# Optimization experiments

Hardware: AMD Instinct MI355X
Metric: run time of the kernel (lower is better)

## Reference

```python
import jax, jax.numpy as jnp
import numpy as np

B, P, K = 8, 2048, 20          # graphs, points per graph, fps samples per graph
N, M = B * P, B * K            # total points, total fps points
C_IN, C_OUT = 64, 128
EPS = 1e-5                     # BatchNorm eps (torch default)


def _linear(x, W, b):
    return x @ W.T + b


def _bn(x, g, b):
    # training-mode BatchNorm1d: batch stats over rows (biased variance)
    m = jnp.mean(x, axis=0)
    v = jnp.var(x, axis=0)
    return g * (x - m) * jax.lax.rsqrt(v + EPS) + b


def _mlp(x, W1, b1, g1, be1, W2, b2, g2, be2):
    h = jax.nn.relu(_bn(_linear(x, W1, b1), g1, be1))
    return jax.nn.relu(_bn(_linear(h, W2, b2), g2, be2))


def setup_inputs() -> dict:
    key = jax.random.key(0)
    ks = jax.random.split(key, 16)
    rng = np.random.default_rng(0)
    # sorted FPS indices: 20 distinct points per graph (matches indices.sort())
    fps = np.sort(rng.choice(P, size=(B, K), replace=False), axis=1)
    fps = fps + np.arange(B)[:, None] * P

    s = 0.05
    inp = {
        "x": jax.random.normal(ks[0], (N, C_IN), jnp.float32),
        "pos": jax.random.normal(ks[1], (N, 3), jnp.float32),
        # q/k/v projections
        "Wq": jax.random.normal(ks[2], (C_OUT, C_IN)) * s, "bq": jnp.zeros((C_OUT,)),
        "Wk": jax.random.normal(ks[3], (C_OUT, C_IN)) * s, "bk": jnp.zeros((C_OUT,)),
        "Wv": jax.random.normal(ks[4], (C_OUT, C_IN)) * s, "bv": jnp.zeros((C_OUT,)),
        # pos MLP: Linear(3,C) BN ReLU Linear(C,C) BN ReLU
        "pW1": jax.random.normal(ks[5], (C_OUT, 3)) * s, "pb1": jnp.zeros((C_OUT,)),
        "pg1": jnp.ones((C_OUT,)), "pbe1": jnp.zeros((C_OUT,)),
        "pW2": jax.random.normal(ks[6], (C_OUT, C_OUT)) * s, "pb2": jnp.zeros((C_OUT,)),
        "pg2": jnp.ones((C_OUT,)), "pbe2": jnp.zeros((C_OUT,)),
        # attn MLP: Linear(C,C) BN ReLU Linear(C,C) BN ReLU
        "aW1": jax.random.normal(ks[7], (C_OUT, C_OUT)) * s, "ab1": jnp.zeros((C_OUT,)),
        "ag1": jnp.ones((C_OUT,)), "abe1": jnp.zeros((C_OUT,)),
        "aW2": jax.random.normal(ks[8], (C_OUT, C_OUT)) * s, "ab2": jnp.zeros((C_OUT,)),
        "ag2": jnp.ones((C_OUT,)), "abe2": jnp.zeros((C_OUT,)),
        "fps_idx": jnp.asarray(fps.reshape(-1), jnp.int32),
        "batch": jnp.repeat(jnp.arange(B, dtype=jnp.int32), P),
    }
    return inp


def reference(x, pos, Wq, bq, Wk, bk, Wv, bv,
              pW1, pb1, pg1, pbe1, pW2, pb2, pg2, pbe2,
              aW1, ab1, ag1, abe1, aW2, ab2, ag2, abe2,
              fps_idx, batch):
    # --- FPS gather + knn(k=1, batched) ---
    fps_pos = pos[fps_idx]                          # [M,3]
    pos_b = pos.reshape(B, P, 3)
    fpos_b = fps_pos.reshape(B, K, 3)
    d2 = jnp.sum((pos_b[:, :, None, :] - fpos_b[:, None, :, :]) ** 2, -1)  # [B,P,K]
    nn_local = jnp.argmin(d2, axis=-1)              # [B,P] nearest fps per point
    e1 = (nn_local + jnp.arange(B)[:, None] * K).reshape(-1)  # [N] global fps idx
    ek1 = 1.0 / (1.0 + 5.0 * jnp.min(d2, axis=-1).reshape(-1))  # [N]

    # --- scatter-mean of kernel-weighted x/pos onto fps nodes ---
    seg = jax.ops.segment_sum
    cnt = jnp.maximum(seg(jnp.ones((N,), x.dtype), e1, num_segments=M), 1.0)[:, None]
    fps_x = seg(ek1[:, None] * x, e1, num_segments=M) / cnt       # [M,C_IN]
    fps_pos = seg(ek1[:, None] * pos, e1, num_segments=M) / cnt   # [M,3]

    # --- q/k/v projections ---
    x_q = _linear(x, Wq, bq)        # [N,C]
    x_k = _linear(fps_x, Wk, bk)    # [M,C]
    x_v = _linear(fps_x, Wv, bv)    # [M,C]

    # --- all-pairs (local point, global fps-in-same-graph) edges: E = N*K ---
    rel = (pos_b[:, :, None, :] - fps_pos.reshape(B, K, 3)[:, None, :, :])
    rel = rel.reshape(N * K, 3)                                   # [E,3]
    delta = _mlp(rel, pW1, pb1, pg1, pbe1, pW2, pb2, pg2, pbe2)   # [E,C]

    qmk = (x_q.reshape(B, P, 1, C_OUT) - x_k.reshape(B, 1, K, C_OUT))
    qmk = qmk.reshape(N * K, C_OUT)                               # [E,C]
    alpha = _mlp(qmk + delta, aW1, ab1, ag1, abe1, aW2, ab2, ag2, abe2)
    # segment softmax over each local point's K edges, per channel
    alpha = jax.nn.softmax(alpha.reshape(B, P, K, C_OUT), axis=2)

    vpd = x_v.reshape(B, 1, K, C_OUT) + delta.reshape(B, P, K, C_OUT)
    out = jnp.sum(vpd * alpha, axis=2).reshape(N, C_OUT)          # scatter-add
    return out
```

## Files before the change

kernel.cpp:

```cpp
#include <hip/hip_runtime.h>
#include <hip/hip_bf16.h>
#include <stdint.h>

#define B_ 8
#define P_ 2048
#define K_ 20
#define N_ (B_*P_)
#define M_ (B_*K_)
#define C 128
#define E_ (N_*K_)
#define EPS_ 1e-5f

typedef unsigned short u16;
typedef unsigned int u32;
typedef __attribute__((ext_vector_type(8))) short short8;
typedef __attribute__((ext_vector_type(4))) float floatx4;

__device__ __forceinline__ float bf2f(u16 u){
    union { u32 i; float f; } v; v.i = ((u32)u) << 16; return v.f;
}
__device__ __forceinline__ u16 f2bf(float f){
    union { float f; u32 i; } v; v.f = f;
    u32 r = ((v.i >> 16) & 1u) + 0x7fffu;
    return (u16)((v.i + r) >> 16);
}
__device__ __forceinline__ u32 pkbf(float a, float b){
    union { __hip_bfloat162 h; u32 u; } cv;
    cv.h = __float22bfloat162_rn(make_float2(a, b));
    return cv.u;
}

__global__ __launch_bounds__(256)
void prep_weights(const float* __restrict__ Wq, const float* __restrict__ bq,
                  const float* __restrict__ Wk, const float* __restrict__ bk,
                  const float* __restrict__ aW1, const float* __restrict__ ab1,
                  const float* __restrict__ pW2, const float* __restrict__ aW2,
                  const float* __restrict__ Wv,
                  float* __restrict__ CqT, float* __restrict__ CkT,
                  float* __restrict__ dq, float* __restrict__ dk,
                  float* __restrict__ WvT,
                  u16* __restrict__ Wb0, u16* __restrict__ Wb1, u16* __restrict__ Wb2)
{
    int tid = threadIdx.x, blk = blockIdx.x;
    if (blk < 32) {
        int idx = blk*256 + tid; int o = idx >> 6, i = idx & 63;
        float s = 0.f;
        for (int cc = 0; cc < 128; ++cc) s = fmaf(aW1[o*128+cc], Wq[cc*64+i], s);
        CqT[i*128 + o] = s;
    } else if (blk < 64) {
        int idx = (blk-32)*256 + tid; int o = idx >> 6, i = idx & 63;
        float s = 0.f;
        for (int cc = 0; cc < 128; ++cc) s = fmaf(aW1[o*128+cc], Wk[cc*64+i], s);
        CkT[i*128 + o] = s;
    } else if (blk == 64) {
        if (tid < 128) {
            float s = ab1[tid];
            for (int cc = 0; cc < 128; ++cc) s = fmaf(aW1[tid*128+cc], bq[cc], s);
            dq[tid] = s;
        } else {
            int o = tid - 128;
            float s = 0.f;
            for (int cc = 0; cc < 128; ++cc) s = fmaf(aW1[o*128+cc], bk[cc], s);
            dk[o] = s;
        }
    } else if (blk == 68) {
        for (int idx = tid; idx < 8192; idx += 256) {
            int o = idx >> 6, i = idx & 63;
            WvT[i*128 + o] = Wv[idx];
        }
    } else {
        const float* src = (blk == 65) ? pW2 : (blk == 66) ? aW1 : aW2;
        u16* dst = (blk == 65) ? Wb0 : (blk == 66) ? Wb1 : Wb2;
        for (int s = tid; s < 2048; s += 256) {
            int ln = s & 63, ks = (s >> 6) & 3, ct = s >> 8;
            int Ls = ln & 15, qs = ln >> 4;
            const float* sp = src + (ct*16+Ls)*C + ks*32 + qs*8;
            #pragma unroll
            for (int j = 0; j < 8; ++j) dst[s*8+j] = f2bf(sp[j]);
        }
    }
}

__global__ __launch_bounds__(256)
void knn_scatter(const float* __restrict__ pos, const float* __restrict__ x,
                 const int* __restrict__ fps_idx, float* __restrict__ gacc,
                 float* __restrict__ posmom)
{
    __shared__ float fpos[K_][3];
    __shared__ float accL[K_*68];
    __shared__ int   skb[64];
    __shared__ float sek[64];
    int tid = threadIdx.x;
    int b = blockIdx.x >> 5;
    if (tid < K_*3) {
        int k = tid / 3, d = tid - k*3;
        fpos[k][d] = pos[fps_idx[b*K_+k]*3 + d];
    }
    for (int i = tid; i < K_*68; i += 256) accL[i] = 0.f;
    __syncthreads();

    int wbase = blockIdx.x*64;
    if (tid < 64) {
        int p = wbase + tid;
        float px = pos[p*3], py = pos[p*3+1], pz = pos[p*3+2];
        float best = 1e30f; int kb = 0;
        #pragma unroll
        for (int k = 0; k < K_; ++k) {
            float dx = px - fpos[k][0], dy = py - fpos[k][1], dz = pz - fpos[k][2];
            float d2 = dx*dx + dy*dy + dz*dz;
            if (d2 < best) { best = d2; kb = k; }
        }
        float ek = 1.0f / (1.0f + 5.0f*best);
        skb[tid] = kb; sek[tid] = ek;
        atomicAdd(&accL[kb*68 + 0], 1.0f);
        atomicAdd(&accL[kb*68 + 1], ek*px);
        atomicAdd(&accL[kb*68 + 2], ek*py);
        atomicAdd(&accL[kb*68 + 3], ek*pz);

        float mom[9] = {px,py,pz, px*px,px*py,px*pz, py*py,py*pz, pz*pz};
        #pragma unroll
        for (int i = 0; i < 9; ++i) {
            float v = mom[i];
            v += __shfl_xor(v,32); v += __shfl_xor(v,16); v += __shfl_xor(v,8);
            v += __shfl_xor(v,4);  v += __shfl_xor(v,2);  v += __shfl_xor(v,1);
            mom[i] = v;
        }
        if (tid == 0) {
            #pragma unroll
            for (int i = 0; i < 9; ++i) atomicAdd(&posmom[b*9+i], mom[i]);
        }
    }
    __syncthreads();

    int w = tid >> 6, lane = tid & 63;
    #pragma unroll
    for (int jj = 0; jj < 16; ++jj) {
        int j = w*16 + jj;
        int   kbj = skb[j];
        float ekj = sek[j];
        float xv = x[(size_t)(wbase+j)*64 + lane];
        atomicAdd(&accL[kbj*68 + 4 + lane], ekj*xv);
    }
    __syncthreads();
    for (int i = tid; i < K_*68; i += 256)
        atomicAdd(&gacc[b*K_*68 + i], accL[i]);
}

__global__ void fps_finalize(float* __restrict__ gacc)
{
    int m = blockIdx.x, t = threadIdx.x;
    float c = gacc[m*68]; c = c > 1.f ? c : 1.f;
    if (t >= 1 && t < 68) gacc[m*68+t] /= c;
}

__global__ __launch_bounds__(256)
void bn1_prep(const float* __restrict__ gacc, const float* __restrict__ posmom,
              const float* __restrict__ pW1, const float* __restrict__ pb1,
              const float* __restrict__ pg1, const float* __restrict__ pbe1,
              float* __restrict__ w3)
{
    __shared__ float sF[8][3], sG[8][6];
    __shared__ float S1[3], S2[6];
    int t = threadIdx.x;
    if (t < 8) {
        float F0=0,F1=0,F2=0,G0=0,G1=0,G2=0,G3=0,G4=0,G5=0;
        for (int k = 0; k < K_; ++k) {
            const float* f = gacc + (t*K_+k)*68 + 1;
            float x=f[0], y=f[1], z=f[2];
            F0+=x; F1+=y; F2+=z;
            G0+=x*x; G1+=x*y; G2+=x*z; G3+=y*y; G4+=y*z; G5+=z*z;
        }
        sF[t][0]=F0; sF[t][1]=F1; sF[t][2]=F2;
        sG[t][0]=G0; sG[t][1]=G1; sG[t][2]=G2; sG[t][3]=G3; sG[t][4]=G4; sG[t][5]=G5;
    }
    __syncthreads();
    if (t == 0) {
        float s1[3]={0,0,0}, s2[6]={0,0,0,0,0,0};
        for (int b = 0; b < 8; ++b) {
            const float* pm = posmom + b*9;
            float Ax=pm[0],Ay=pm[1],Az=pm[2];
            float Fx=sF[b][0],Fy=sF[b][1],Fz=sF[b][2];
            s1[0] += (float)K_*Ax - (float)P_*Fx;
            s1[1] += (float)K_*Ay - (float)P_*Fy;
            s1[2] += (float)K_*Az - (float)P_*Fz;
            s2[0] += (float)K_*pm[3] - 2.f*Ax*Fx + (float)P_*sG[b][0];
            s2[1] += (float)K_*pm[4] - Ax*Fy - Ay*Fx + (float)P_*sG[b][1];
            s2[2] += (float)K_*pm[5] - Ax*Fz - Az*Fx + (float)P_*sG[b][2];
            s2[3] += (float)K_*pm[6] - 2.f*Ay*Fy + (float)P_*sG[b][3];
            s2[4] += (float)K_*pm[7] - Ay*Fz - Az*Fy + (float)P_*sG[b][4];
            s2[5] += (float)K_*pm[8] - 2.f*Az*Fz + (float)P_*sG[b][5];
        }
        for (int i = 0; i < 3; ++i) S1[i] = s1[i];
        for (int i = 0; i < 6; ++i) S2[i] = s2[i];
    }
    __syncthreads();
    if (t < 128) {
        float w0=pW1[t*3], w1=pW1[t*3+1], w2=pW1[t*3+2], bb=pb1[t];
        float wS1 = w0*S1[0] + w1*S1[1] + w2*S1[2];
        float wS2w = w0*w0*S2[0] + w1*w1*S2[3] + w2*w2*S2[5]
                   + 2.f*(w0*w1*S2[1] + w0*w2*S2[2] + w1*w2*S2[4]);
        const float invE = 1.0f/(float)E_;
        float m1  = wS1*invE + bb;
        float Ez2 = (wS2w + 2.f*bb*wS1)*invE + bb*bb;
        float var = Ez2 - m1*m1;
        float sc = pg1[t] * rsqrtf(var + EPS_);
        float sh = pbe1[t] - m1*sc;
        w3[0*128+t] = w0*sc; w3[1*128+t] = w1*sc;
        w3[2*128+t] = w2*sc; w3[3*128+t] = bb*sc + sh;
    }
}

__global__ __launch_bounds__(128)
void proj_m(const float* __restrict__ gacc, const float* __restrict__ CkT,
            const float* __restrict__ dk, const float* __restrict__ WvT,
            const float* __restrict__ bv, float* __restrict__ Ak2,
            float* __restrict__ xv)
{
    int m = blockIdx.x, o = threadIdx.x;
    const float* fx = gacc + m*68 + 4;
    float a = dk[o], v = bv[o];
    for (int i = 0; i < 64; ++i) {
        float xi = fx[i];
        a = fmaf(CkT[i*128+o], xi, a);
        v = fmaf(WvT[i*128+o], xi, v);
    }
    Ak2[m*C+o] = a; xv[m*C+o] = v;
}

__global__ __launch_bounds__(256)
void proj_q(const float* __restrict__ x, const float* __restrict__ CqT,
            const float* __restrict__ dq, float* __restrict__ Aq2)
{
    __shared__ float xs[512];
    int tid = threadIdx.x;
    int p0 = blockIdx.x*8;
    const float* xp = x + (size_t)p0*64;
    for (int i = tid; i < 512; i += 256) xs[i] = xp[i];
    __syncthreads();
    int g = tid >> 7, o = tid & 127;
    const float* xb = xs + g*256;
    float d = dq[o];
    float a0=d, a1=d, a2=d, a3=d;
    #pragma unroll 4
    for (int i = 0; i < 64; ++i) {
        float w = CqT[i*128 + o];
        a0 = fmaf(w, xb[i],       a0);
        a1 = fmaf(w, xb[64+i],    a1);
        a2 = fmaf(w, xb[128+i],   a2);
        a3 = fmaf(w, xb[192+i],   a3);
    }
    int pb = p0 + g*4;
    Aq2[(size_t)(pb+0)*C + o] = a0;
    Aq2[(size_t)(pb+1)*C + o] = a1;
    Aq2[(size_t)(pb+2)*C + o] = a2;
    Aq2[(size_t)(pb+3)*C + o] = a3;
}

__global__ __launch_bounds__(256)
void finalize_stats(const float* __restrict__ stats32,
                    const float* __restrict__ g, const float* __restrict__ be,
                    float* __restrict__ scale, float* __restrict__ shift)
{
    __shared__ float red[256];
    int tid = threadIdx.x;
    float s = 0.f;
    for (int r = 0; r < 32; ++r) s += stats32[r*256 + tid];
    red[tid] = s;
    __syncthreads();
    if (tid < C) {
        float mean = red[tid] * (1.0f/E_);
        float var  = red[C+tid] * (1.0f/E_) - mean*mean;
        float sc = g[tid] * rsqrtf(var + EPS_);
        scale[tid] = sc;
        shift[tid] = be[tid] - mean*sc;
    }
}

template<int MODE>
__global__ __launch_bounds__(256)
void gemm_fused(const u16* __restrict__ zin, u16* __restrict__ zout,
                const u16* __restrict__ Wbf,
                const float* __restrict__ scale, const float* __restrict__ shift,
                const float* __restrict__ w3,
                const float* __restrict__ bias,
                const float* __restrict__ rowq, const float* __restrict__ rowk,
                const float* __restrict__ pos, const float* __restrict__ gacc,
                float* __restrict__ stats32)
{
    __shared__ float s_stat[2][C];
    __shared__ float saff[5*C];

    int tid = threadIdx.x;
    const int wave = tid >> 6, lane = tid & 63;
    const int L = lane & 15, q = lane >> 4;

    ((float*)s_stat)[tid] = 0.f;
    if constexpr (MODE == 0) {
        for (int i = tid; i < 512; i += 256) saff[i] = w3[i];
        if (tid < C) saff[512+tid] = bias[tid];
    } else {
        if (tid < C) { saff[tid] = scale[tid]; saff[C+tid] = shift[tid]; }
        if constexpr (MODE == 2) { if (tid < C) saff[2*C+tid] = bias[tid]; }
    }
    __syncthreads();

    int tbs[2];
    tbs[0] = (blockIdx.x*8 + wave)*16;
    tbs[1] = (blockIdx.x*8 + wave + 4)*16;

    short8 An[2][4];
    float rr0[2], rr1[2], rr2[2];
    #pragma unroll
    for (int tt = 0; tt < 2; ++tt) {
        if constexpr (MODE != 0) {
            const u16* ap = zin + (size_t)(tbs[tt] + L)*C + q*8;
            An[tt][0] = *(const short8*)ap;
            An[tt][1] = *(const short8*)(ap + 32);
            An[tt][2] = *(const short8*)(ap + 64);
            An[tt][3] = *(const short8*)(ap + 96);
        } else {
            unsigned e = (unsigned)(tbs[tt] + L);
            unsigned p = e / 20u; int k = (int)(e - p*20u);
            int m = (int)(p >> 11)*20 + k;
            const float* fp = gacc + m*68 + 1;
            rr0[tt] = pos[p*3]   - fp[0];
            rr1[tt] = pos[p*3+1] - fp[1];
            rr2[tt] = pos[p*3+2] - fp[2];
        }
    }

    floatx4 acc[2][8];
    #pragma unroll
    for (int tt = 0; tt < 2; ++tt)
        #pragma unroll
        for (int ct = 0; ct < 8; ++ct) acc[tt][ct] = (floatx4){0.f,0.f,0.f,0.f};

    #pragma unroll
    for (int ks = 0; ks < 4; ++ks) {
        int ch0 = ks*32 + q*8;
        short8 bfr[8];
        #pragma unroll
        for (int ct = 0; ct < 8; ++ct)
            bfr[ct] = *(const short8*)(Wbf + ((ct*4+ks)*64 + lane)*8);
        #pragma unroll
        for (int tt = 0; tt < 2; ++tt) {
            union { short8 s8; u32 u[4]; } af;
            if constexpr (MODE == 0) {
                #pragma unroll
                for (int jj = 0; jj < 4; ++jj) {
                    int c0 = ch0 + jj*2, c1 = ch0 + jj*2 + 1;
                    float f0 = fmaf(saff[c0], rr0[tt], fmaf(saff[C+c0], rr1[tt],
                               fmaf(saff[2*C+c0], rr2[tt], saff[3*C+c0])));
                    float f1 = fmaf(saff[c1], rr0[tt], fmaf(saff[C+c1], rr1[tt],
                               fmaf(saff[2*C+c1], rr2[tt], saff[3*C+c1])));
                    f0 = f0 > 0.f ? f0 : 0.f;
                    f1 = f1 > 0.f ? f1 : 0.f;
                    af.u[jj] = pkbf(f0, f1);
                }
            } else {
                short8 ar = An[tt][ks];
                #pragma unroll
                for (int jj = 0; jj < 4; ++jj) {
                    int c0 = ch0 + jj*2, c1 = ch0 + jj*2 + 1;
                    float f0 = fmaf(bf2f((u16)ar[jj*2]),   saff[c0], saff[C+c0]);
                    float f1 = fmaf(bf2f((u16)ar[jj*2+1]), saff[c1], saff[C+c1]);
                    f0 = f0 > 0.f ? f0 : 0.f;
                    f1 = f1 > 0.f ? f1 : 0.f;
                    af.u[jj] = pkbf(f0, f1);
                }
            }
            #pragma unroll
            for (int ct = 0; ct < 8; ++ct)
                acc[tt][ct] = __builtin_amdgcn_mfma_f32_16x16x32_bf16(af.s8, bfr[ct], acc[tt][ct], 0, 0, 0);
        }
    }

    float ssum[8], ssq[8];
    #pragma unroll
    for (int i = 0; i < 8; ++i) { ssum[i] = 0.f; ssq[i] = 0.f; }

    #pragma unroll
    for (int tt = 0; tt < 2; ++tt) {
        const int tilebase = tbs[tt];
        int pp[4], mm[4];
        if constexpr (MODE == 1) {
            #pragma unroll
            for (int r = 0; r < 4; ++r) {
                unsigned e2 = (unsigned)(tilebase + q*4 + r);
                unsigned p2 = e2 / 20u; int k2 = (int)(e2 - p2*20u);
                pp[r] = (int)p2; mm[r] = (int)(p2 >> 11)*20 + k2;
            }
        }
        u16* orow = zout + (size_t)(tilebase + q*4)*C + L;
        #pragma unroll
        for (int ct = 0; ct < 8; ++ct) {
            int col = ct*16 + L;
            float bb;
            if constexpr (MODE == 0) bb = saff[4*C + col];
            else if constexpr (MODE == 2) bb = saff[2*C + col];
            else bb = 0.f;
            #pragma unroll
            for (int r = 0; r < 4; ++r) {
                float z = acc[tt][ct][r] + bb;
                if constexpr (MODE == 1)
                    z += rowq[pp[r]*C + col] - rowk[mm[r]*C + col];
                ssum[ct] += z; ssq[ct] += z*z;
                orow[(size_t)r*C + ct*16] = (u16)pkbf(z, z);
            }
        }
    }

    #pragma unroll
    for (int ct = 0; ct < 8; ++ct) {
        float v = ssum[ct]; v += __shfl_xor(v,16); v += __shfl_xor(v,32);
        float w = ssq[ct];  w += __shfl_xor(w,16); w += __shfl_xor(w,32);
        if (lane < 16) {
            atomicAdd(&s_stat[0][ct*16+L], v);
            atomicAdd(&s_stat[1][ct*16+L], w);
        }
    }
    __syncthreads();
    float* dst = stats32 + ((blockIdx.x & 31) << 8);
    atomicAdd(&dst[tid], ((float*)s_stat)[tid]);
}

__global__ __launch_bounds__(256)
void final_kernel(const u16* __restrict__ z2, const u16* __restrict__ za2,
                  const float* __restrict__ sc2, const float* __restrict__ sh2,
                  const float* __restrict__ sc4, const float* __restrict__ sh4,
                  const float* __restrict__ xv, float* __restrict__ out)
{
    int tid = threadIdx.x;
    int p = blockIdx.x*4 + (tid >> 6);
    int lane = tid & 63;
    int c2 = lane*2;
    int b = p >> 11;
    float S2x=sc2[c2], S2y=sc2[c2+1], H2x=sh2[c2], H2y=sh2[c2+1];
    float S4x=sc4[c2], S4y=sc4[c2+1], H4x=sh4[c2], H4y=sh4[c2+1];
    size_t ebase = (size_t)p * K_;
    const float* xvb = xv + (size_t)(b*K_)*C + c2;
    float l0 = 0.f, l1 = 0.f, o0 = 0.f, o1 = 0.f;
    #pragma unroll
    for (int k = 0; k < K_; ++k) {
        u32 wa = *(const u32*)(za2 + (ebase+k)*C + c2);
        u32 wz = *(const u32*)(z2  + (ebase+k)*C + c2);
        float2 xvv = *(const float2*)(xvb + (size_t)k*C);
        float aa0 = fmaf(bf2f((u16)(wa & 0xffffu)), S4x, H4x); aa0 = aa0 > 0.f ? aa0 : 0.f;
        float aa1 = fmaf(bf2f((u16)(wa >> 16)),     S4y, H4y); aa1 = aa1 > 0.f ? aa1 : 0.f;
        float dd0 = fmaf(bf2f((u16)(wz & 0xffffu)), S2x, H2x); dd0 = dd0 > 0.f ? dd0 : 0.f;
        float dd1 = fmaf(bf2f((u16)(wz >> 16)),     S2y, H2y); dd1 = dd1 > 0.f ? dd1 : 0.f;
        float e0 = __expf(aa0), e1 = __expf(aa1);
        l0 += e0; l1 += e1;
        o0 = fmaf(e0, xvv.x + dd0, o0);
        o1 = fmaf(e1, xvv.y + dd1, o1);
    }
    out[(size_t)p*C + c2]     = o0 / l0;
    out[(size_t)p*C + c2 + 1] = o1 / l1;
}

extern "C" void kernel_launch(void* const* d_in, const int* in_sizes, int n_in,
                              void* d_out, int out_size, void* d_ws, size_t ws_size,
                              hipStream_t stream)
{
    const float* x    = (const float*)d_in[0];
    const float* pos  = (const float*)d_in[1];
    const float* Wq   = (const float*)d_in[2];
    const float* bq   = (const float*)d_in[3];
    const float* Wk   = (const float*)d_in[4];
    const float* bk   = (const float*)d_in[5];
    const float* Wv   = (const float*)d_in[6];
    const float* bv   = (const float*)d_in[7];
    const float* pW1  = (const float*)d_in[8];
    const float* pb1  = (const float*)d_in[9];
    const float* pg1  = (const float*)d_in[10];
    const float* pbe1 = (const float*)d_in[11];
    const float* pW2  = (const float*)d_in[12];
    const float* pb2  = (const float*)d_in[13];
    const float* pg2  = (const float*)d_in[14];
    const float* pbe2 = (const float*)d_in[15];
    const float* aW1  = (const float*)d_in[16];
    const float* ab1  = (const float*)d_in[17];
    const float* ag1  = (const float*)d_in[18];
    const float* abe1 = (const float*)d_in[19];
    const float* aW2  = (const float*)d_in[20];
    const float* ab2  = (const float*)d_in[21];
    const float* ag2  = (const float*)d_in[22];
    const float* abe2 = (const float*)d_in[23];
    const int* fps_idx = (const int*)d_in[24];
    float* out = (float*)d_out;

    char* ws = (char*)d_ws;
    size_t off = 0;
    auto alloc = [&](size_t bytes) -> void* {
        void* r = ws + off;
        off = (off + bytes + 255) & ~(size_t)255;
        return r;
    };
    float* gacc    = (float*)alloc(160*68*4);
    float* posmom  = (float*)alloc(8*9*4);
    float* stats32 = (float*)alloc(3*32*256*4);
    size_t zero_bytes = off;
    float* aff = (float*)alloc(6*128*4);
    float* w3  = (float*)alloc(4*128*4);
    float* CqT = (float*)alloc(64*128*4);
    float* CkT = (float*)alloc(64*128*4);
    float* dq  = (float*)alloc(128*4);
    float* dk  = (float*)alloc(128*4);
    float* WvT = (float*)alloc(64*128*4);
    u16* Wb0   = (u16*)alloc(128*128*2);
    u16* Wb1   = (u16*)alloc(128*128*2);
    u16* Wb2   = (u16*)alloc(128*128*2);
    float* Aq2 = (float*)alloc((size_t)N_*128*4);
    float* Ak2 = (float*)alloc(160*128*4);
    float* xv  = (float*)alloc(160*128*4);
    u16* bigA  = (u16*)alloc((size_t)E_*128*2);
    u16* bigB  = (u16*)alloc((size_t)E_*128*2);

    hipMemsetAsync(d_ws, 0, zero_bytes, stream);

    prep_weights<<<69, 256, 0, stream>>>(Wq, bq, Wk, bk, aW1, ab1, pW2, aW2, Wv,
                                         CqT, CkT, dq, dk, WvT, Wb0, Wb1, Wb2);
    knn_scatter<<<256, 256, 0, stream>>>(pos, x, fps_idx, gacc, posmom);
    fps_finalize<<<160, 128, 0, stream>>>(gacc);
    bn1_prep<<<1, 256, 0, stream>>>(gacc, posmom, pW1, pb1, pg1, pbe1, w3);
    proj_m<<<160, 128, 0, stream>>>(gacc, CkT, dk, WvT, bv, Ak2, xv);
    proj_q<<<N_/8, 256, 0, stream>>>(x, CqT, dq, Aq2);

    float* stA = stats32;
    float* stB = stats32 + 32*256;
    float* stC = stats32 + 2*32*256;

    gemm_fused<0><<<E_/128, 256, 0, stream>>>(nullptr, bigA, Wb0,
        nullptr, nullptr, w3, pb2, nullptr, nullptr, pos, gacc, stA);
    finalize_stats<<<1, 256, 0, stream>>>(stA, pg2, pbe2, aff + 0, aff + 128);

    gemm_fused<1><<<E_/128, 256, 0, stream>>>(bigA, bigB, Wb1,
        aff + 0, aff + 128, nullptr, nullptr, Aq2, Ak2, nullptr, nullptr, stB);
    finalize_stats<<<1, 256, 0, stream>>>(stB, ag1, abe1, aff + 256, aff + 384);

    gemm_fused<2><<<E_/128, 256, 0, stream>>>(bigB, bigB, Wb2,
        aff + 256, aff + 384, nullptr, ab2, nullptr, nullptr, nullptr, nullptr, stC);
    finalize_stats<<<1, 256, 0, stream>>>(stC, ag2, abe2, aff + 512, aff + 640);

    final_kernel<<<N_/4, 256, 0, stream>>>(bigA, bigB, aff + 0, aff + 128,
                                           aff + 512, aff + 640, xv, out);
}
```

Before: 333.7 us.

## Fold BN stat finalization into consumers and recompute last GEMM in final kernel

Removes the separate finalize_stats and fps_finalize launches by computing BatchNorm scale/shift inside each consuming kernel and normalizing fps features inside proj_m. The third GEMM becomes a stats-only pass (MODE 3) that no longer writes its bf16 output, and the final kernel recomputes that GEMM with MFMA and fuses it with the softmax-weighted aggregation. This trades an extra full GEMM pass plus redundant per-block stat reductions for skipping a large intermediate write/read and several small launches.

```diff
diff --git a/kernel.cpp b/kernel.cpp
--- a/kernel.cpp
+++ b/kernel.cpp
@@ -138,19 +138,37 @@
         int j = w*16 + jj;
         int   kbj = skb[j];
         float ekj = sek[j];
-        float xv = x[(size_t)(wbase+j)*64 + lane];
-        atomicAdd(&accL[kbj*68 + 4 + lane], ekj*xv);
+        float xvv = x[(size_t)(wbase+j)*64 + lane];
+        atomicAdd(&accL[kbj*68 + 4 + lane], ekj*xvv);
     }
     __syncthreads();
     for (int i = tid; i < K_*68; i += 256)
         atomicAdd(&gacc[b*K_*68 + i], accL[i]);
 }
 
-__global__ void fps_finalize(float* __restrict__ gacc)
-{
-    int m = blockIdx.x, t = threadIdx.x;
-    float c = gacc[m*68]; c = c > 1.f ? c : 1.f;
-    if (t >= 1 && t < 68) gacc[m*68+t] /= c;
+__global__ __launch_bounds__(128)
+void proj_m(float* __restrict__ gacc, const float* __restrict__ CkT,
+            const float* __restrict__ dk, const float* __restrict__ WvT,
+            const float* __restrict__ bv, float* __restrict__ Ak2,
+            float* __restrict__ xv)
+{
+    __shared__ float sfx[68];
+    int m = blockIdx.x, o = threadIdx.x;
+    if (o < 68) {
+        float c = gacc[m*68];
+        float inv = 1.0f / (c > 1.f ? c : 1.f);
+        float vdiv = (o >= 1) ? gacc[m*68+o]*inv : c;
+        sfx[o] = vdiv;
+        if (o >= 1) gacc[m*68+o] = vdiv;
+    }
+    __syncthreads();
+    float a = dk[o], v = bv[o];
+    for (int i = 0; i < 64; ++i) {
+        float xi = sfx[4+i];
+        a = fmaf(CkT[i*128+o], xi, a);
+        v = fmaf(WvT[i*128+o], xi, v);
+    }
+    Ak2[m*C+o] = a; xv[m*C+o] = v;
 }
 
 __global__ __launch_bounds__(256)
@@ -210,23 +228,6 @@
     }
 }
 
-__global__ __launch_bounds__(128)
-void proj_m(const float* __restrict__ gacc, const float* __restrict__ CkT,
-            const float* __restrict__ dk, const float* __restrict__ WvT,
-            const float* __restrict__ bv, float* __restrict__ Ak2,
-            float* __restrict__ xv)
-{
-    int m = blockIdx.x, o = threadIdx.x;
-    const float* fx = gacc + m*68 + 4;
-    float a = dk[o], v = bv[o];
-    for (int i = 0; i < 64; ++i) {
-        float xi = fx[i];
-        a = fmaf(CkT[i*128+o], xi, a);
-        v = fmaf(WvT[i*128+o], xi, v);
-    }
-    Ak2[m*C+o] = a; xv[m*C+o] = v;
-}
-
 __global__ __launch_bounds__(256)
 void proj_q(const float* __restrict__ x, const float* __restrict__ CqT,
             const float* __restrict__ dq, float* __restrict__ Aq2)
@@ -256,33 +257,13 @@
     Aq2[(size_t)(pb+3)*C + o] = a3;
 }
 
-__global__ __launch_bounds__(256)
-void finalize_stats(const float* __restrict__ stats32,
-                    const float* __restrict__ g, const float* __restrict__ be,
-                    float* __restrict__ scale, float* __restrict__ shift)
-{
-    __shared__ float red[256];
-    int tid = threadIdx.x;
-    float s = 0.f;
-    for (int r = 0; r < 32; ++r) s += stats32[r*256 + tid];
-    red[tid] = s;
-    __syncthreads();
-    if (tid < C) {
-        float mean = red[tid] * (1.0f/E_);
-        float var  = red[C+tid] * (1.0f/E_) - mean*mean;
-        float sc = g[tid] * rsqrtf(var + EPS_);
-        scale[tid] = sc;
-        shift[tid] = be[tid] - mean*sc;
-    }
-}
-
 template<int MODE>
 __global__ __launch_bounds__(256)
 void gemm_fused(const u16* __restrict__ zin, u16* __restrict__ zout,
                 const u16* __restrict__ Wbf,
-                const float* __restrict__ scale, const float* __restrict__ shift,
-                const float* __restrict__ w3,
-                const float* __restrict__ bias,
+                const float* __restrict__ statsin, const float* __restrict__ g,
+                const float* __restrict__ be,
+                const float* __restrict__ w3, const float* __restrict__ bias,
                 const float* __restrict__ rowq, const float* __restrict__ rowk,
                 const float* __restrict__ pos, const float* __restrict__ gacc,
                 float* __restrict__ stats32)
@@ -299,8 +280,19 @@
         for (int i = tid; i < 512; i += 256) saff[i] = w3[i];
         if (tid < C) saff[512+tid] = bias[tid];
     } else {
-        if (tid < C) { saff[tid] = scale[tid]; saff[C+tid] = shift[tid]; }
-        if constexpr (MODE == 2) { if (tid < C) saff[2*C+tid] = bias[tid]; }
+        if (tid < C) {
+            float s = 0.f, sq = 0.f;
+            for (int r = 0; r < 32; ++r) {
+                s  += statsin[r*256 + tid];
+                sq += statsin[r*256 + 128 + tid];
+            }
+            float mean = s*(1.0f/E_), var = sq*(1.0f/E_) - mean*mean;
+            float sc = g[tid] * rsqrtf(var + EPS_);
+            saff[tid] = sc; saff[C+tid] = be[tid] - mean*sc;
+        }
+        if constexpr (MODE == 3) {
+            if (tid >= 128) saff[2*C + tid - 128] = bias[tid - 128];
+        }
     }
     __syncthreads();
 
@@ -391,13 +383,13 @@
                 pp[r] = (int)p2; mm[r] = (int)(p2 >> 11)*20 + k2;
             }
         }
-        u16* orow = zout + (size_t)(tilebase + q*4)*C + L;
+        u16* orow = (MODE != 3) ? (zout + (size_t)(tilebase + q*4)*C + L) : nullptr;
         #pragma unroll
         for (int ct = 0; ct < 8; ++ct) {
             int col = ct*16 + L;
             float bb;
             if constexpr (MODE == 0) bb = saff[4*C + col];
-            else if constexpr (MODE == 2) bb = saff[2*C + col];
+            else if constexpr (MODE == 3) bb = saff[2*C + col];
             else bb = 0.f;
             #pragma unroll
             for (int r = 0; r < 4; ++r) {
@@ -405,7 +397,8 @@
                 if constexpr (MODE == 1)
                     z += rowq[pp[r]*C + col] - rowk[mm[r]*C + col];
                 ssum[ct] += z; ssq[ct] += z*z;
-                orow[(size_t)r*C + ct*16] = (u16)pkbf(z, z);
+                if constexpr (MODE != 3)
+                    orow[(size_t)r*C + ct*16] = (u16)pkbf(z, z);
             }
         }
     }
@@ -425,37 +418,137 @@
 }
 
 __global__ __launch_bounds__(256)
-void final_kernel(const u16* __restrict__ z2, const u16* __restrict__ za2,
-                  const float* __restrict__ sc2, const float* __restrict__ sh2,
-                  const float* __restrict__ sc4, const float* __restrict__ sh4,
-                  const float* __restrict__ xv, float* __restrict__ out)
-{
+void final_fused(const u16* __restrict__ z2, const u16* __restrict__ za1,
+                 const u16* __restrict__ Wbf,
+                 const float* __restrict__ stA, const float* __restrict__ pg2,
+                 const float* __restrict__ pbe2,
+                 const float* __restrict__ stB, const float* __restrict__ ag1,
+                 const float* __restrict__ abe1,
+                 const float* __restrict__ stC, const float* __restrict__ ag2,
+                 const float* __restrict__ abe2,
+                 const float* __restrict__ ab2, const float* __restrict__ xv,
+                 float* __restrict__ out)
+{
+    __shared__ float saff[7*C];
+    __shared__ float sxv[20*132];
     int tid = threadIdx.x;
-    int p = blockIdx.x*4 + (tid >> 6);
-    int lane = tid & 63;
-    int c2 = lane*2;
-    int b = p >> 11;
-    float S2x=sc2[c2], S2y=sc2[c2+1], H2x=sh2[c2], H2y=sh2[c2+1];
-    float S4x=sc4[c2], S4y=sc4[c2+1], H4x=sh4[c2], H4y=sh4[c2+1];
-    size_t ebase = (size_t)p * K_;
-    const float* xvb = xv + (size_t)(b*K_)*C + c2;
-    float l0 = 0.f, l1 = 0.f, o0 = 0.f, o1 = 0.f;
-    #pragma unroll
-    for (int k = 0; k < K_; ++k) {
-        u32 wa = *(const u32*)(za2 + (ebase+k)*C + c2);
-        u32 wz = *(const u32*)(z2  + (ebase+k)*C + c2);
-        float2 xvv = *(const float2*)(xvb + (size_t)k*C);
-        float aa0 = fmaf(bf2f((u16)(wa & 0xffffu)), S4x, H4x); aa0 = aa0 > 0.f ? aa0 : 0.f;
-        float aa1 = fmaf(bf2f((u16)(wa >> 16)),     S4y, H4y); aa1 = aa1 > 0.f ? aa1 : 0.f;
-        float dd0 = fmaf(bf2f((u16)(wz & 0xffffu)), S2x, H2x); dd0 = dd0 > 0.f ? dd0 : 0.f;
-        float dd1 = fmaf(bf2f((u16)(wz >> 16)),     S2y, H2y); dd1 = dd1 > 0.f ? dd1 : 0.f;
-        float e0 = __expf(aa0), e1 = __expf(aa1);
-        l0 += e0; l1 += e1;
-        o0 = fmaf(e0, xvv.x + dd0, o0);
-        o1 = fmaf(e1, xvv.y + dd1, o1);
-    }
-    out[(size_t)p*C + c2]     = o0 / l0;
-    out[(size_t)p*C + c2 + 1] = o1 / l1;
+    if (tid < C) {
+        float s=0.f, sq=0.f;
+        for (int r = 0; r < 32; ++r) { s += stB[r*256+tid]; sq += stB[r*256+128+tid]; }
+        float mean = s*(1.0f/E_), var = sq*(1.0f/E_)-mean*mean;
+        float sc = ag1[tid]*rsqrtf(var+EPS_);
+        saff[tid] = sc; saff[C+tid] = abe1[tid]-mean*sc;
+        s=0.f; sq=0.f;
+        for (int r = 0; r < 32; ++r) { s += stA[r*256+tid]; sq += stA[r*256+128+tid]; }
+        mean = s*(1.0f/E_); var = sq*(1.0f/E_)-mean*mean;
+        sc = pg2[tid]*rsqrtf(var+EPS_);
+        saff[4*C+tid] = sc; saff[5*C+tid] = pbe2[tid]-mean*sc;
+    } else {
+        int c = tid - C;
+        float s=0.f, sq=0.f;
+        for (int r = 0; r < 32; ++r) { s += stC[r*256+c]; sq += stC[r*256+128+c]; }
+        float mean = s*(1.0f/E_), var = sq*(1.0f/E_)-mean*mean;
+        float sc = ag2[c]*rsqrtf(var+EPS_);
+        saff[2*C+c] = sc; saff[3*C+c] = abe2[c]-mean*sc;
+        saff[6*C+c] = ab2[c];
+    }
+    int w = tid >> 6, lane = tid & 63;
+    int p0blk = blockIdx.x * 16;
+    int graph = p0blk >> 11;
+    const float* xvg = xv + (size_t)graph*20*C;
+    for (int i = tid; i < 20*C; i += 256) sxv[(i>>7)*132 + (i&127)] = xvg[i];
+    __syncthreads();
+
+    const int L = lane & 15, q = lane >> 4;
+    const int wavebase = blockIdx.x*320 + w*80;
+    const int p0 = p0blk + w*4;
+
+    float num[4][8], den[4][8];
+    #pragma unroll
+    for (int a = 0; a < 4; ++a)
+        #pragma unroll
+        for (int c = 0; c < 8; ++c) { num[a][c] = 0.f; den[a][c] = 0.f; }
+
+    const int lpA_t[5]    = {0, 0, 1, 2, 3};
+    const int rsplit_t[5] = {16, 4, 8, 12, 16};
+
+    #pragma unroll
+    for (int t = 0; t < 5; ++t) {
+        const int tilebase = wavebase + t*16;
+        const u16* ap = za1 + (size_t)(tilebase + L)*C + q*8;
+        short8 Ar[4];
+        Ar[0] = *(const short8*)ap;
+        Ar[1] = *(const short8*)(ap + 32);
+        Ar[2] = *(const short8*)(ap + 64);
+        Ar[3] = *(const short8*)(ap + 96);
+
+        floatx4 acc[8];
+        #pragma unroll
+        for (int ct = 0; ct < 8; ++ct) acc[ct] = (floatx4){0.f,0.f,0.f,0.f};
+
+        #pragma unroll
+        for (int ks = 0; ks < 4; ++ks) {
+            int ch0 = ks*32 + q*8;
+            short8 ar = Ar[ks];
+            union { short8 s8; u32 u[4]; } af;
+            #pragma unroll
+            for (int jj = 0; jj < 4; ++jj) {
+                int c0 = ch0 + jj*2, c1 = ch0 + jj*2 + 1;
+                float f0 = fmaf(bf2f((u16)ar[jj*2]),   saff[c0], saff[C+c0]);
+                float f1 = fmaf(bf2f((u16)ar[jj*2+1]), saff[c1], saff[C+c1]);
+                f0 = f0 > 0.f ? f0 : 0.f;
+                f1 = f1 > 0.f ? f1 : 0.f;
+                af.u[jj] = pkbf(f0, f1);
+            }
+            #pragma unroll
+            for (int ct = 0; ct < 8; ++ct) {
+                short8 bfr = *(const short8*)(Wbf + ((ct*4+ks)*64 + lane)*8);
+                acc[ct] = __builtin_amdgcn_mfma_f32_16x16x32_bf16(af.s8, bfr, acc[ct], 0, 0, 0);
+            }
+        }
+
+        const int lpA = lpA_t[t], rs = rsplit_t[t];
+        #pragma unroll
+        for (int ct = 0; ct < 8; ++ct) {
+            int col = ct*16 + L;
+            float sc4v = saff[2*C+col], sh4v = saff[3*C+col];
+            float sc2v = saff[4*C+col], sh2v = saff[5*C+col];
+            float bb   = saff[6*C+col];
+            float eA = 0.f, evA = 0.f, eB = 0.f, evB = 0.f;
+            #pragma unroll
+            for (int r = 0; r < 4; ++r) {
+                int rloc = q*4 + r;
+                int row = tilebase + rloc;
+                float za2v = acc[ct][r] + bb;
+                float a = fmaf(sc4v, za2v, sh4v); a = a > 0.f ? a : 0.f;
+                float e_ = __expf(a);
+                float zz = bf2f(z2[(size_t)row*C + col]);
+                float dd = fmaf(sc2v, zz, sh2v); dd = dd > 0.f ? dd : 0.f;
+                bool isB = rloc >= rs;
+                int lp = isB ? lpA + 1 : lpA;
+                int k  = t*16 + rloc - 20*lp;
+                float v = sxv[k*132 + col] + dd;
+                if (isB) { eB += e_; evB += e_*v; }
+                else     { eA += e_; evA += e_*v; }
+            }
+            num[lpA][ct] += evA; den[lpA][ct] += eA;
+            if (rs < 16) { num[lpA+1][ct] += evB; den[lpA+1][ct] += eB; }
+        }
+    }
+
+    #pragma unroll
+    for (int a = 0; a < 4; ++a)
+        #pragma unroll
+        for (int c = 0; c < 8; ++c) {
+            float n = num[a][c], d = den[a][c];
+            n += __shfl_xor(n, 16); n += __shfl_xor(n, 32);
+            d += __shfl_xor(d, 16); d += __shfl_xor(d, 32);
+            num[a][c] = n; den[a][c] = d;
+        }
+    float* op = out + (size_t)(p0 + q)*C + L;
+    #pragma unroll
+    for (int c = 0; c < 8; ++c)
+        op[c*16] = num[q][c] / den[q][c];
 }
 
 extern "C" void kernel_launch(void* const* d_in, const int* in_sizes, int n_in,
@@ -500,7 +593,6 @@
     float* posmom  = (float*)alloc(8*9*4);
     float* stats32 = (float*)alloc(3*32*256*4);
     size_t zero_bytes = off;
-    float* aff = (float*)alloc(6*128*4);
     float* w3  = (float*)alloc(4*128*4);
     float* CqT = (float*)alloc(64*128*4);
     float* CkT = (float*)alloc(64*128*4);
@@ -521,9 +613,8 @@
     prep_weights<<<69, 256, 0, stream>>>(Wq, bq, Wk, bk, aW1, ab1, pW2, aW2, Wv,
                                          CqT, CkT, dq, dk, WvT, Wb0, Wb1, Wb2);
     knn_scatter<<<256, 256, 0, stream>>>(pos, x, fps_idx, gacc, posmom);
-    fps_finalize<<<160, 128, 0, stream>>>(gacc);
+    proj_m<<<160, 128, 0, stream>>>(gacc, CkT, dk, WvT, bv, Ak2, xv);
     bn1_prep<<<1, 256, 0, stream>>>(gacc, posmom, pW1, pb1, pg1, pbe1, w3);
-    proj_m<<<160, 128, 0, stream>>>(gacc, CkT, dk, WvT, bv, Ak2, xv);
     proj_q<<<N_/8, 256, 0, stream>>>(x, CqT, dq, Aq2);
 
     float* stA = stats32;
@@ -531,17 +622,14 @@
     float* stC = stats32 + 2*32*256;
 
     gemm_fused<0><<<E_/128, 256, 0, stream>>>(nullptr, bigA, Wb0,
-        nullptr, nullptr, w3, pb2, nullptr, nullptr, pos, gacc, stA);
-    finalize_stats<<<1, 256, 0, stream>>>(stA, pg2, pbe2, aff + 0, aff + 128);
+        nullptr, nullptr, nullptr, w3, pb2, nullptr, nullptr, pos, gacc, stA);
 
     gemm_fused<1><<<E_/128, 256, 0, stream>>>(bigA, bigB, Wb1,
-        aff + 0, aff + 128, nullptr, nullptr, Aq2, Ak2, nullptr, nullptr, stB);
-    finalize_stats<<<1, 256, 0, stream>>>(stB, ag1, abe1, aff + 256, aff + 384);
-
-    gemm_fused<2><<<E_/128, 256, 0, stream>>>(bigB, bigB, Wb2,
-        aff + 256, aff + 384, nullptr, ab2, nullptr, nullptr, nullptr, nullptr, stC);
-    finalize_stats<<<1, 256, 0, stream>>>(stC, ag2, abe2, aff + 512, aff + 640);
-
-    final_kernel<<<N_/4, 256, 0, stream>>>(bigA, bigB, aff + 0, aff + 128,
-                                           aff + 512, aff + 640, xv, out);
-}
+        stA, pg2, pbe2, nullptr, nullptr, Aq2, Ak2, nullptr, nullptr, stB);
+
+    gemm_fused<3><<<E_/128, 256, 0, stream>>>(bigB, nullptr, Wb2,
+        stB, ag1, abe1, nullptr, ab2, nullptr, nullptr, nullptr, nullptr, stC);
+
+    final_fused<<<N_/16, 256, 0, stream>>>(bigA, bigB, Wb2,
+        stA, pg2, pbe2, stB, ag1, abe1, stC, ag2, abe2, ab2, xv, out);
+}
```

Measured after the change: 491.1 us. 1.47x slower.

## Fold BN stat finalization and fps normalization into consumer kernels

Applied to the files above, without the earlier changes.

Removes the fps_finalize kernel by doing the count division inside proj_m, which is launched before bn1_prep so that gacc is already normalized when bn1_prep reads it. Removes three single-block finalize_stats launches by having each gemm_fused block and each final_kernel block rebuild BN scale and shift from the 32-row partial stats. Output stores in gemm_fused become nontemporal. This cuts launch count and serial tiny kernels, at the cost of redundant per-block reduction work and possibly worse cache behaviour for intermediates that are read back soon after being written.

```diff
diff --git a/kernel.cpp b/kernel.cpp
--- a/kernel.cpp
+++ b/kernel.cpp
@@ -138,19 +138,37 @@
         int j = w*16 + jj;
         int   kbj = skb[j];
         float ekj = sek[j];
-        float xv = x[(size_t)(wbase+j)*64 + lane];
-        atomicAdd(&accL[kbj*68 + 4 + lane], ekj*xv);
+        float xvv = x[(size_t)(wbase+j)*64 + lane];
+        atomicAdd(&accL[kbj*68 + 4 + lane], ekj*xvv);
     }
     __syncthreads();
     for (int i = tid; i < K_*68; i += 256)
         atomicAdd(&gacc[b*K_*68 + i], accL[i]);
 }
 
-__global__ void fps_finalize(float* __restrict__ gacc)
-{
-    int m = blockIdx.x, t = threadIdx.x;
-    float c = gacc[m*68]; c = c > 1.f ? c : 1.f;
-    if (t >= 1 && t < 68) gacc[m*68+t] /= c;
+__global__ __launch_bounds__(128)
+void proj_m(float* __restrict__ gacc, const float* __restrict__ CkT,
+            const float* __restrict__ dk, const float* __restrict__ WvT,
+            const float* __restrict__ bv, float* __restrict__ Ak2,
+            float* __restrict__ xv)
+{
+    __shared__ float sfx[68];
+    int m = blockIdx.x, o = threadIdx.x;
+    if (o < 68) {
+        float c = gacc[m*68];
+        float inv = 1.0f / (c > 1.f ? c : 1.f);
+        float vdiv = (o >= 1) ? gacc[m*68+o]*inv : c;
+        sfx[o] = vdiv;
+        if (o >= 1) gacc[m*68+o] = vdiv;
+    }
+    __syncthreads();
+    float a = dk[o], v = bv[o];
+    for (int i = 0; i < 64; ++i) {
+        float xi = sfx[4+i];
+        a = fmaf(CkT[i*128+o], xi, a);
+        v = fmaf(WvT[i*128+o], xi, v);
+    }
+    Ak2[m*C+o] = a; xv[m*C+o] = v;
 }
 
 __global__ __launch_bounds__(256)
@@ -210,23 +228,6 @@
     }
 }
 
-__global__ __launch_bounds__(128)
-void proj_m(const float* __restrict__ gacc, const float* __restrict__ CkT,
-            const float* __restrict__ dk, const float* __restrict__ WvT,
-            const float* __restrict__ bv, float* __restrict__ Ak2,
-            float* __restrict__ xv)
-{
-    int m = blockIdx.x, o = threadIdx.x;
-    const float* fx = gacc + m*68 + 4;
-    float a = dk[o], v = bv[o];
-    for (int i = 0; i < 64; ++i) {
-        float xi = fx[i];
-        a = fmaf(CkT[i*128+o], xi, a);
-        v = fmaf(WvT[i*128+o], xi, v);
-    }
-    Ak2[m*C+o] = a; xv[m*C+o] = v;
-}
-
 __global__ __launch_bounds__(256)
 void proj_q(const float* __restrict__ x, const float* __restrict__ CqT,
             const float* __restrict__ dq, float* __restrict__ Aq2)
@@ -256,33 +257,13 @@
     Aq2[(size_t)(pb+3)*C + o] = a3;
 }
 
-__global__ __launch_bounds__(256)
-void finalize_stats(const float* __restrict__ stats32,
-                    const float* __restrict__ g, const float* __restrict__ be,
-                    float* __restrict__ scale, float* __restrict__ shift)
-{
-    __shared__ float red[256];
-    int tid = threadIdx.x;
-    float s = 0.f;
-    for (int r = 0; r < 32; ++r) s += stats32[r*256 + tid];
-    red[tid] = s;
-    __syncthreads();
-    if (tid < C) {
-        float mean = red[tid] * (1.0f/E_);
-        float var  = red[C+tid] * (1.0f/E_) - mean*mean;
-        float sc = g[tid] * rsqrtf(var + EPS_);
-        scale[tid] = sc;
-        shift[tid] = be[tid] - mean*sc;
-    }
-}
-
 template<int MODE>
 __global__ __launch_bounds__(256)
 void gemm_fused(const u16* __restrict__ zin, u16* __restrict__ zout,
                 const u16* __restrict__ Wbf,
-                const float* __restrict__ scale, const float* __restrict__ shift,
-                const float* __restrict__ w3,
-                const float* __restrict__ bias,
+                const float* __restrict__ statsin, const float* __restrict__ g,
+                const float* __restrict__ be,
+                const float* __restrict__ w3, const float* __restrict__ bias,
                 const float* __restrict__ rowq, const float* __restrict__ rowk,
                 const float* __restrict__ pos, const float* __restrict__ gacc,
                 float* __restrict__ stats32)
@@ -299,8 +280,19 @@
         for (int i = tid; i < 512; i += 256) saff[i] = w3[i];
         if (tid < C) saff[512+tid] = bias[tid];
     } else {
-        if (tid < C) { saff[tid] = scale[tid]; saff[C+tid] = shift[tid]; }
-        if constexpr (MODE == 2) { if (tid < C) saff[2*C+tid] = bias[tid]; }
+        if (tid < C) {
+            float s = 0.f, sq = 0.f;
+            for (int r = 0; r < 32; ++r) {
+                s  += statsin[r*256 + tid];
+                sq += statsin[r*256 + 128 + tid];
+            }
+            float mean = s*(1.0f/E_), var = sq*(1.0f/E_) - mean*mean;
+            float sc = g[tid] * rsqrtf(var + EPS_);
+            saff[tid] = sc; saff[C+tid] = be[tid] - mean*sc;
+        }
+        if constexpr (MODE == 2) {
+            if (tid >= 128) saff[2*C + tid - 128] = bias[tid - 128];
+        }
     }
     __syncthreads();
 
@@ -405,7 +397,8 @@
                 if constexpr (MODE == 1)
                     z += rowq[pp[r]*C + col] - rowk[mm[r]*C + col];
                 ssum[ct] += z; ssq[ct] += z*z;
-                orow[(size_t)r*C + ct*16] = (u16)pkbf(z, z);
+                __builtin_nontemporal_store((u16)pkbf(z, z),
+                                            &orow[(size_t)r*C + ct*16]);
             }
         }
     }
@@ -426,17 +419,36 @@
 
 __global__ __launch_bounds__(256)
 void final_kernel(const u16* __restrict__ z2, const u16* __restrict__ za2,
-                  const float* __restrict__ sc2, const float* __restrict__ sh2,
-                  const float* __restrict__ sc4, const float* __restrict__ sh4,
+                  const float* __restrict__ stA, const float* __restrict__ pg2,
+                  const float* __restrict__ pbe2,
+                  const float* __restrict__ stC, const float* __restrict__ ag2,
+                  const float* __restrict__ abe2,
                   const float* __restrict__ xv, float* __restrict__ out)
 {
+    __shared__ float saff[4*C];
     int tid = threadIdx.x;
+    if (tid < C) {
+        float s=0.f, sq=0.f;
+        for (int r = 0; r < 32; ++r) { s += stA[r*256+tid]; sq += stA[r*256+128+tid]; }
+        float mean = s*(1.0f/E_), var = sq*(1.0f/E_)-mean*mean;
+        float sc = pg2[tid]*rsqrtf(var+EPS_);
+        saff[tid] = sc; saff[C+tid] = pbe2[tid]-mean*sc;
+    } else {
+        int c = tid - C;
+        float s=0.f, sq=0.f;
+        for (int r = 0; r < 32; ++r) { s += stC[r*256+c]; sq += stC[r*256+128+c]; }
+        float mean = s*(1.0f/E_), var = sq*(1.0f/E_)-mean*mean;
+        float sc = ag2[c]*rsqrtf(var+EPS_);
+        saff[2*C+c] = sc; saff[3*C+c] = abe2[c]-mean*sc;
+    }
+    __syncthreads();
+
     int p = blockIdx.x*4 + (tid >> 6);
     int lane = tid & 63;
     int c2 = lane*2;
     int b = p >> 11;
-    float S2x=sc2[c2], S2y=sc2[c2+1], H2x=sh2[c2], H2y=sh2[c2+1];
-    float S4x=sc4[c2], S4y=sc4[c2+1], H4x=sh4[c2], H4y=sh4[c2+1];
+    float S2x=saff[c2], S2y=saff[c2+1], H2x=saff[C+c2], H2y=saff[C+c2+1];
+    float S4x=saff[2*C+c2], S4y=saff[2*C+c2+1], H4x=saff[3*C+c2], H4y=saff[3*C+c2+1];
     size_t ebase = (size_t)p * K_;
     const float* xvb = xv + (size_t)(b*K_)*C + c2;
     float l0 = 0.f, l1 = 0.f, o0 = 0.f, o1 = 0.f;
@@ -500,7 +512,6 @@
     float* posmom  = (float*)alloc(8*9*4);
     float* stats32 = (float*)alloc(3*32*256*4);
     size_t zero_bytes = off;
-    float* aff = (float*)alloc(6*128*4);
     float* w3  = (float*)alloc(4*128*4);
     float* CqT = (float*)alloc(64*128*4);
     float* CkT = (float*)alloc(64*128*4);
@@ -521,9 +532,8 @@
     prep_weights<<<69, 256, 0, stream>>>(Wq, bq, Wk, bk, aW1, ab1, pW2, aW2, Wv,
                                          CqT, CkT, dq, dk, WvT, Wb0, Wb1, Wb2);
     knn_scatter<<<256, 256, 0, stream>>>(pos, x, fps_idx, gacc, posmom);
-    fps_finalize<<<160, 128, 0, stream>>>(gacc);
+    proj_m<<<160, 128, 0, stream>>>(gacc, CkT, dk, WvT, bv, Ak2, xv);
     bn1_prep<<<1, 256, 0, stream>>>(gacc, posmom, pW1, pb1, pg1, pbe1, w3);
-    proj_m<<<160, 128, 0, stream>>>(gacc, CkT, dk, WvT, bv, Ak2, xv);
     proj_q<<<N_/8, 256, 0, stream>>>(x, CqT, dq, Aq2);
 
     float* stA = stats32;
@@ -531,17 +541,14 @@
     float* stC = stats32 + 2*32*256;
 
     gemm_fused<0><<<E_/128, 256, 0, stream>>>(nullptr, bigA, Wb0,
-        nullptr, nullptr, w3, pb2, nullptr, nullptr, pos, gacc, stA);
-    finalize_stats<<<1, 256, 0, stream>>>(stA, pg2, pbe2, aff + 0, aff + 128);
+        nullptr, nullptr, nullptr, w3, pb2, nullptr, nullptr, pos, gacc, stA);
 
     gemm_fused<1><<<E_/128, 256, 0, stream>>>(bigA, bigB, Wb1,
-        aff + 0, aff + 128, nullptr, nullptr, Aq2, Ak2, nullptr, nullptr, stB);
-    finalize_stats<<<1, 256, 0, stream>>>(stB, ag1, abe1, aff + 256, aff + 384);
+        stA, pg2, pbe2, nullptr, nullptr, Aq2, Ak2, nullptr, nullptr, stB);
 
     gemm_fused<2><<<E_/128, 256, 0, stream>>>(bigB, bigB, Wb2,
-        aff + 256, aff + 384, nullptr, ab2, nullptr, nullptr, nullptr, nullptr, stC);
-    finalize_stats<<<1, 256, 0, stream>>>(stC, ag2, abe2, aff + 512, aff + 640);
-
-    final_kernel<<<N_/4, 256, 0, stream>>>(bigA, bigB, aff + 0, aff + 128,
-                                           aff + 512, aff + 640, xv, out);
-}
+        stB, ag1, abe1, nullptr, ab2, nullptr, nullptr, nullptr, nullptr, stC);
+
+    final_kernel<<<N_/4, 256, 0, stream>>>(bigA, bigB,
+        stA, pg2, pbe2, stC, ag2, abe2, xv, out);
+}
```

Result: slower. 365.9 us (+9.6%).
